# Performance work log

Measured on AMD Instinct MI355X. Metric: run time of the kernel, lower is better.

## Reference

```python
import jax, jax.numpy as jnp
import numpy as np

K = 3          # kernel size
STRIDE = 1
PAD = 1
DIL = 1


def setup_inputs() -> dict:
    key = jax.random.key(0)
    k1, k2, k3 = jax.random.split(key, 3)
    N, Cin, H, W = 8, 128, 64, 64
    Cout = 128
    x = jax.random.normal(k1, (N, Cin, H, W), dtype=jnp.float32)
    # offset channels: 2 * deformable_groups * K*K = 18, interleaved (dy, dx) per tap
    offset = jax.random.normal(k2, (N, 2 * K * K, H, W), dtype=jnp.float32)
    weight = jax.random.normal(k3, (Cout, Cin, K, K), dtype=jnp.float32) / np.sqrt(Cin * K * K)
    return {"x": x, "offset": offset, "weight": weight}


def _deform_conv(x, offset, weight):
    N, Cin, H, W = x.shape
    Cout = weight.shape[0]
    KK = K * K
    Ho, Wo = offset.shape[2], offset.shape[3]

    off = offset.reshape(N, KK, 2, Ho, Wo)
    dy = off[:, :, 0]  # [N, KK, Ho, Wo]
    dx = off[:, :, 1]

    kh = jnp.repeat(jnp.arange(K), K).astype(x.dtype)   # [KK]
    kw = jnp.tile(jnp.arange(K), K).astype(x.dtype)     # [KK]
    base_i = (jnp.arange(Ho) * STRIDE - PAD).astype(x.dtype)  # [Ho]
    base_j = (jnp.arange(Wo) * STRIDE - PAD).astype(x.dtype)  # [Wo]

    # Sampling positions: [N, KK, Ho, Wo]
    py = base_i[None, None, :, None] + (kh * DIL)[None, :, None, None] + dy
    px = base_j[None, None, None, :] + (kw * DIL)[None, :, None, None] + dx

    y0 = jnp.floor(py)
    x0 = jnp.floor(px)
    wy1 = py - y0
    wx1 = px - x0
    wy0 = 1.0 - wy1
    wx0 = 1.0 - wx1
    y0i = y0.astype(jnp.int32)
    x0i = x0.astype(jnp.int32)
    y1i = y0i + 1
    x1i = x0i + 1

    x_flat = x.reshape(N, Cin, H * W)

    def gather(yi, xi):
        # zero-padding outside the image
        mask = ((yi >= 0) & (yi < H) & (xi >= 0) & (xi < W)).astype(x.dtype)
        idx = jnp.clip(yi, 0, H - 1) * W + jnp.clip(xi, 0, W - 1)  # [N,KK,Ho,Wo]
        v = jnp.take_along_axis(x_flat, idx.reshape(N, 1, -1), axis=2)  # [N,Cin,KK*Ho*Wo]
        v = v.reshape(N, Cin, KK, Ho, Wo)
        return v * mask[:, None]

    sampled = (gather(y0i, x0i) * (wy0 * wx0)[:, None]
               + gather(y0i, x1i) * (wy0 * wx1)[:, None]
               + gather(y1i, x0i) * (wy1 * wx0)[:, None]
               + gather(y1i, x1i) * (wy1 * wx1)[:, None])  # [N,Cin,KK,Ho,Wo]

    w = weight.reshape(Cout, Cin, KK)
    return jnp.einsum('nckij,ock->noij', sampled, w)


def reference(x, offset, weight):
    return _deform_conv(x, offset, weight)
```

## Files before the change

kernel.cpp:

```cpp
#include <hip/hip_runtime.h>


#define H  64
#define W  64
#define CIN 128
#define COUT 128
#define NB 8
#define KK 9

typedef short bf16x8 __attribute__((ext_vector_type(8)));
typedef float f32x4  __attribute__((ext_vector_type(4)));
typedef __attribute__((address_space(3))) unsigned int lds_u32;
typedef __attribute__((address_space(1))) const unsigned int gbl_u32;

__device__ __forceinline__ unsigned short f2bf(float f) {
    unsigned u = __builtin_bit_cast(unsigned, f);
    u += 0x7FFFu + ((u >> 16) & 1u);
    return (unsigned short)(u >> 16);
}
__device__ __forceinline__ float lo_f(unsigned u) { return __builtin_bit_cast(float, u << 16); }
__device__ __forceinline__ float hi_f(unsigned u) { return __builtin_bit_cast(float, u & 0xFFFF0000u); }

__global__ void prep_all(const float* __restrict__ x, const float* __restrict__ w,
                         unsigned short* __restrict__ xt, unsigned short* __restrict__ wtf) {
    if (blockIdx.x < 72) {
        int id = blockIdx.x * 256 + threadIdx.x;
        int lane = id & 63;
        int ct = (id >> 6) & 3;
        int nt = (id >> 8) & 7;
        int kk = id >> 11;
        int co = nt * 16 + (lane & 15);
        int c0 = ct * 32 + (lane >> 4) * 8;
        unsigned short v[8];
        #pragma unroll
        for (int j = 0; j < 8; ++j)
            v[j] = f2bf(w[((size_t)co * CIN + c0 + j) * KK + kk]);
        *(uint4*)(wtf + (size_t)id * 8) = *(const uint4*)v;
    }
    __shared__ float tile[CIN][W + 1];
    int b = blockIdx.x;
    int n = b >> 6, y = b & 63;
    int t = threadIdx.x;
    int l = t & 63, g = t >> 6;
    const float* src = x + ((size_t)n * CIN * H + y) * W;
    #pragma unroll
    for (int i = 0; i < 32; ++i) {
        int c = g * 32 + i;
        tile[c][l] = src[(size_t)c * H * W + l];
    }
    __syncthreads();
    int xp = t & 63;
    int cb = (t >> 6) * 32;
    unsigned short* dst = xt + (((size_t)(n * H + y) * W + xp) * CIN + cb);
    unsigned rr[16];
    #pragma unroll
    for (int i = 0; i < 16; ++i) {
        rr[i] = (unsigned)f2bf(tile[cb + 2 * i][xp])
              | ((unsigned)f2bf(tile[cb + 2 * i + 1][xp]) << 16);
    }
    #pragma unroll
    for (int i = 0; i < 4; ++i)
        ((uint4*)dst)[i] = make_uint4(rr[4*i], rr[4*i+1], rr[4*i+2], rr[4*i+3]);
}

__global__ __launch_bounds__(256, 3) void deform_main(
        const float* __restrict__ offs, const unsigned short* __restrict__ xt,
        const unsigned short* __restrict__ wtf, float* __restrict__ out) {
    __shared__ __attribute__((aligned(16))) char lds_raw[50176];
    unsigned short* samp = (unsigned short*)lds_raw;
    unsigned short* wts  = (unsigned short*)(lds_raw + 17408);
    float* ot            = (float*)lds_raw;

    int b = blockIdx.x;
    int n = b >> 6, ho = b & 63;
    int t = threadIdx.x;
    int lane = t & 63, wv = t >> 6;
    int lm = lane & 15, lq = lane >> 4;

    int p  = t >> 2;
    int cb = (t & 3) << 5;
    const float* offp = offs + (((size_t)n * 2 * KK) * H + ho) * W + p;
    const unsigned short* xbase = xt + (size_t)n * H * W * CIN + cb;

    f32x4 acc[8] = {};

    float dy = offp[0];
    float dx = offp[(size_t)H * W];
    int kh = 0, kw = 0;
    for (int kk = 0; kk < KK; ++kk) {
        {
            const unsigned short* gb = wtf + (size_t)kk * 16384 + wv * 4096;
            unsigned short* lb = wts + wv * 4096;
            #pragma unroll
            for (int i = 0; i < 8; ++i)
                __builtin_amdgcn_global_load_lds((gbl_u32*)(gb + i * 512 + lane * 8),
                                                 (lds_u32*)(lb + i * 512), 16, 0, 0);
        }
        float py = (float)(ho - 1 + kh) + dy;
        float px = (float)(p  - 1 + kw) + dx;
        float y0f = floorf(py), x0f = floorf(px);
        float wy1 = py - y0f, wx1 = px - x0f;
        float wy0 = 1.f - wy1, wx0 = 1.f - wx1;
        int y0 = (int)y0f, x0 = (int)x0f;
        int y1 = y0 + 1, x1 = x0 + 1;
        bool vy0 = (unsigned)y0 < (unsigned)H, vy1 = (unsigned)y1 < (unsigned)H;
        bool vx0 = (unsigned)x0 < (unsigned)W, vx1 = (unsigned)x1 < (unsigned)W;
        float w00 = (vy0 && vx0) ? wy0 * wx0 : 0.f;
        float w01 = (vy0 && vx1) ? wy0 * wx1 : 0.f;
        float w10 = (vy1 && vx0) ? wy1 * wx0 : 0.f;
        float w11 = (vy1 && vx1) ? wy1 * wx1 : 0.f;
        int yc0 = min(max(y0, 0), H - 1), yc1 = min(max(y1, 0), H - 1);
        int xc0 = min(max(x0, 0), W - 1), xc1 = min(max(x1, 0), W - 1);
        const unsigned short* r0 = xbase + (size_t)yc0 * (W * CIN);
        const unsigned short* r1 = xbase + (size_t)yc1 * (W * CIN);
        const unsigned short* b00 = r0 + (xc0 << 7);
        const unsigned short* b01 = r0 + (xc1 << 7);
        const unsigned short* b10 = r1 + (xc0 << 7);
        const unsigned short* b11 = r1 + (xc1 << 7);
        unsigned short* sdst = samp + p * 136 + cb;
        #pragma unroll
        for (int j = 0; j < 4; ++j) {
            uint4 q00 = *(const uint4*)(b00 + 8 * j);
            uint4 q01 = *(const uint4*)(b01 + 8 * j);
            uint4 q10 = *(const uint4*)(b10 + 8 * j);
            uint4 q11 = *(const uint4*)(b11 + 8 * j);
            const unsigned* a0 = (const unsigned*)&q00;
            const unsigned* a1 = (const unsigned*)&q01;
            const unsigned* a2 = (const unsigned*)&q10;
            const unsigned* a3 = (const unsigned*)&q11;
            unsigned rr[4];
            #pragma unroll
            for (int i = 0; i < 4; ++i) {
                float v0 = w00*lo_f(a0[i]) + w01*lo_f(a1[i]) + w10*lo_f(a2[i]) + w11*lo_f(a3[i]);
                float v1 = w00*hi_f(a0[i]) + w01*hi_f(a1[i]) + w10*hi_f(a2[i]) + w11*hi_f(a3[i]);
                rr[i] = (unsigned)f2bf(v0) | ((unsigned)f2bf(v1) << 16);
            }
            *(uint4*)(sdst + 8 * j) = make_uint4(rr[0], rr[1], rr[2], rr[3]);
        }
        if (kk < KK - 1) {
            dy = offp[(size_t)(2 * kk + 2) * H * W];
            dx = offp[(size_t)(2 * kk + 3) * H * W];
        }
        ++kw; if (kw == 3) { kw = 0; ++kh; }
        __syncthreads();
        const unsigned short* arow = samp + (wv * 16 + lm) * 136 + (lq << 3);
        const unsigned short* bbase = wts + (lane << 3);
        #pragma unroll
        for (int ct = 0; ct < 4; ++ct) {
            bf16x8 a = *(const bf16x8*)(arow + (ct << 5));
            #pragma unroll
            for (int nt = 0; nt < 8; ++nt) {
                bf16x8 bf = *(const bf16x8*)(bbase + ((nt << 2) + ct) * 512);
                acc[nt] = __builtin_amdgcn_mfma_f32_16x16x32_bf16(a, bf, acc[nt], 0, 0, 0);
            }
        }
        __syncthreads();
    }
    #pragma unroll
    for (int nt = 0; nt < 8; ++nt) {
        float* orow = ot + (nt * 16 + lm) * 65 + wv * 16 + (lq << 2);
        orow[0] = acc[nt][0]; orow[1] = acc[nt][1];
        orow[2] = acc[nt][2]; orow[3] = acc[nt][3];
    }
    __syncthreads();
    int co2 = t >> 1, wo2 = (t & 1) << 5;
    const float* srow = ot + co2 * 65 + wo2;
    float* dstg = out + (((size_t)(n * COUT + co2) * H + ho) * W + wo2);
    #pragma unroll
    for (int i = 0; i < 8; ++i) {
        f32x4 v = { srow[4*i], srow[4*i+1], srow[4*i+2], srow[4*i+3] };
        *(f32x4*)(dstg + 4 * i) = v;
    }
}

extern "C" void kernel_launch(void* const* d_in, const int* in_sizes, int n_in,
                              void* d_out, int out_size, void* d_ws, size_t ws_size,
                              hipStream_t stream) {
    const float* x      = (const float*)d_in[0];
    const float* offset = (const float*)d_in[1];
    const float* weight = (const float*)d_in[2];
    float* out = (float*)d_out;

    unsigned short* xt  = (unsigned short*)d_ws;
    unsigned short* wtf = (unsigned short*)((char*)d_ws + (size_t)NB*H*W*CIN*2);

    hipLaunchKernelGGL(prep_all, dim3(NB * H), dim3(256), 0, stream, x, weight, xt, wtf);
    hipLaunchKernelGGL(deform_main, dim3(NB * H), dim3(256), 0, stream,
                       offset, xt, wtf, out);
}
```

Measured before the change: 121.6 us.

## Sample bilinear values directly into MFMA A-fragments, removing LDS staging

Each lane now computes bilinear samples for exactly the pixel and channel slice it feeds as its MFMA A operand, so the sampled tile never passes through LDS. Weights are read straight from global/L2 as B fragments instead of being staged with global_load_lds, and outputs go straight from accumulators to global memory. All __syncthreads and the LDS buffer disappear, which removes barrier stalls and LDS traffic. The costs are more global weight loads per wave, a larger register footprint (occupancy hint lowered to 2), and output stores that are less coalesced.

```diff
diff --git a/kernel.cpp b/kernel.cpp
--- a/kernel.cpp
+++ b/kernel.cpp
@@ -10,8 +10,6 @@
 
 typedef short bf16x8 __attribute__((ext_vector_type(8)));
 typedef float f32x4  __attribute__((ext_vector_type(4)));
-typedef __attribute__((address_space(3))) unsigned int lds_u32;
-typedef __attribute__((address_space(1))) const unsigned int gbl_u32;
 
 __device__ __forceinline__ unsigned short f2bf(float f) {
     unsigned u = __builtin_bit_cast(unsigned, f);
@@ -63,39 +61,25 @@
         ((uint4*)dst)[i] = make_uint4(rr[4*i], rr[4*i+1], rr[4*i+2], rr[4*i+3]);
 }
 
-__global__ __launch_bounds__(256, 3) void deform_main(
+__global__ __launch_bounds__(256, 2) void deform_main(
         const float* __restrict__ offs, const unsigned short* __restrict__ xt,
         const unsigned short* __restrict__ wtf, float* __restrict__ out) {
-    __shared__ __attribute__((aligned(16))) char lds_raw[50176];
-    unsigned short* samp = (unsigned short*)lds_raw;
-    unsigned short* wts  = (unsigned short*)(lds_raw + 17408);
-    float* ot            = (float*)lds_raw;
-
     int b = blockIdx.x;
     int n = b >> 6, ho = b & 63;
     int t = threadIdx.x;
     int lane = t & 63, wv = t >> 6;
     int lm = lane & 15, lq = lane >> 4;
+    int p = (wv << 4) + lm;
+    int cb0 = lq << 3;
 
-    int p  = t >> 2;
-    int cb = (t & 3) << 5;
     const float* offp = offs + (((size_t)n * 2 * KK) * H + ho) * W + p;
-    const unsigned short* xbase = xt + (size_t)n * H * W * CIN + cb;
+    const unsigned short* xbase = xt + (size_t)n * H * W * CIN + cb0;
 
     f32x4 acc[8] = {};
-
     float dy = offp[0];
     float dx = offp[(size_t)H * W];
     int kh = 0, kw = 0;
     for (int kk = 0; kk < KK; ++kk) {
-        {
-            const unsigned short* gb = wtf + (size_t)kk * 16384 + wv * 4096;
-            unsigned short* lb = wts + wv * 4096;
-            #pragma unroll
-            for (int i = 0; i < 8; ++i)
-                __builtin_amdgcn_global_load_lds((gbl_u32*)(gb + i * 512 + lane * 8),
-                                                 (lds_u32*)(lb + i * 512), 16, 0, 0);
-        }
         float py = (float)(ho - 1 + kh) + dy;
         float px = (float)(p  - 1 + kw) + dx;
         float y0f = floorf(py), x0f = floorf(px);
@@ -111,23 +95,30 @@
         float w11 = (vy1 && vx1) ? wy1 * wx1 : 0.f;
         int yc0 = min(max(y0, 0), H - 1), yc1 = min(max(y1, 0), H - 1);
         int xc0 = min(max(x0, 0), W - 1), xc1 = min(max(x1, 0), W - 1);
-        const unsigned short* r0 = xbase + (size_t)yc0 * (W * CIN);
-        const unsigned short* r1 = xbase + (size_t)yc1 * (W * CIN);
-        const unsigned short* b00 = r0 + (xc0 << 7);
-        const unsigned short* b01 = r0 + (xc1 << 7);
-        const unsigned short* b10 = r1 + (xc0 << 7);
-        const unsigned short* b11 = r1 + (xc1 << 7);
-        unsigned short* sdst = samp + p * 136 + cb;
+        const unsigned short* c00 = xbase + ((yc0 * W + xc0) << 7);
+        const unsigned short* c01 = xbase + ((yc0 * W + xc1) << 7);
+        const unsigned short* c10 = xbase + ((yc1 * W + xc0) << 7);
+        const unsigned short* c11 = xbase + ((yc1 * W + xc1) << 7);
+        uint4 q[4][4];
         #pragma unroll
-        for (int j = 0; j < 4; ++j) {
-            uint4 q00 = *(const uint4*)(b00 + 8 * j);
-            uint4 q01 = *(const uint4*)(b01 + 8 * j);
-            uint4 q10 = *(const uint4*)(b10 + 8 * j);
-            uint4 q11 = *(const uint4*)(b11 + 8 * j);
-            const unsigned* a0 = (const unsigned*)&q00;
-            const unsigned* a1 = (const unsigned*)&q01;
-            const unsigned* a2 = (const unsigned*)&q10;
-            const unsigned* a3 = (const unsigned*)&q11;
+        for (int ct = 0; ct < 4; ++ct) {
+            q[ct][0] = *(const uint4*)(c00 + (ct << 5));
+            q[ct][1] = *(const uint4*)(c01 + (ct << 5));
+            q[ct][2] = *(const uint4*)(c10 + (ct << 5));
+            q[ct][3] = *(const uint4*)(c11 + (ct << 5));
+        }
+        if (kk < KK - 1) {
+            dy = offp[(size_t)(2 * kk + 2) * H * W];
+            dx = offp[(size_t)(2 * kk + 3) * H * W];
+        }
+        ++kw; if (kw == 3) { kw = 0; ++kh; }
+        const unsigned short* wk = wtf + (size_t)kk * 16384 + (lane << 3);
+        #pragma unroll
+        for (int ct = 0; ct < 4; ++ct) {
+            const unsigned* a0 = (const unsigned*)&q[ct][0];
+            const unsigned* a1 = (const unsigned*)&q[ct][1];
+            const unsigned* a2 = (const unsigned*)&q[ct][2];
+            const unsigned* a3 = (const unsigned*)&q[ct][3];
             unsigned rr[4];
             #pragma unroll
             for (int i = 0; i < 4; ++i) {
@@ -135,41 +126,19 @@
                 float v1 = w00*hi_f(a0[i]) + w01*hi_f(a1[i]) + w10*hi_f(a2[i]) + w11*hi_f(a3[i]);
                 rr[i] = (unsigned)f2bf(v0) | ((unsigned)f2bf(v1) << 16);
             }
-            *(uint4*)(sdst + 8 * j) = make_uint4(rr[0], rr[1], rr[2], rr[3]);
-        }
-        if (kk < KK - 1) {
-            dy = offp[(size_t)(2 * kk + 2) * H * W];
-            dx = offp[(size_t)(2 * kk + 3) * H * W];
-        }
-        ++kw; if (kw == 3) { kw = 0; ++kh; }
-        __syncthreads();
-        const unsigned short* arow = samp + (wv * 16 + lm) * 136 + (lq << 3);
-        const unsigned short* bbase = wts + (lane << 3);
-        #pragma unroll
-        for (int ct = 0; ct < 4; ++ct) {
-            bf16x8 a = *(const bf16x8*)(arow + (ct << 5));
+            bf16x8 a = __builtin_bit_cast(bf16x8, *(uint4*)rr);
             #pragma unroll
             for (int nt = 0; nt < 8; ++nt) {
-                bf16x8 bf = *(const bf16x8*)(bbase + ((nt << 2) + ct) * 512);
+                bf16x8 bf = *(const bf16x8*)(wk + (((nt << 2) + ct) << 9));
                 acc[nt] = __builtin_amdgcn_mfma_f32_16x16x32_bf16(a, bf, acc[nt], 0, 0, 0);
             }
         }
-        __syncthreads();
     }
+    int wo = (wv << 4) + (lq << 2);
     #pragma unroll
     for (int nt = 0; nt < 8; ++nt) {
-        float* orow = ot + (nt * 16 + lm) * 65 + wv * 16 + (lq << 2);
-        orow[0] = acc[nt][0]; orow[1] = acc[nt][1];
-        orow[2] = acc[nt][2]; orow[3] = acc[nt][3];
-    }
-    __syncthreads();
-    int co2 = t >> 1, wo2 = (t & 1) << 5;
-    const float* srow = ot + co2 * 65 + wo2;
-    float* dstg = out + (((size_t)(n * COUT + co2) * H + ho) * W + wo2);
-    #pragma unroll
-    for (int i = 0; i < 8; ++i) {
-        f32x4 v = { srow[4*i], srow[4*i+1], srow[4*i+2], srow[4*i+3] };
-        *(f32x4*)(dstg + 4 * i) = v;
+        int co = (nt << 4) + lm;
+        *(f32x4*)(out + (((size_t)(n * COUT + co) * H + ho) * W + wo)) = acc[nt];
     }
 }
 
```

Result: slower. 127.3 us (+4.8%).
